# Kernel tuning notes

Hardware: AMD Instinct MI355X
Metric: run time of the kernel (lower is better)

Reference implementation:

```python
import jax, jax.numpy as jnp
import numpy as np

N = 10000       # nodes
E = 200000      # node pairs (edges) in rel_dict
R = 400000      # relation instances
F_IN = 128
F_OUT = 64


def setup_inputs() -> dict:
    key = jax.random.key(0)
    ks = jax.random.split(key, 8)
    x = jax.random.normal(ks[0], (N, F_IN), dtype=jnp.float32)
    rel = jax.random.normal(ks[1], (R, F_IN), dtype=jnp.float32)
    adj = jax.random.uniform(ks[2], (N, N), dtype=jnp.float32)
    edge_pairs = jax.random.randint(ks[3], (E, 2), 0, N, dtype=jnp.int32)
    rel_seg = jax.random.randint(ks[4], (R,), 0, E, dtype=jnp.int32)
    # Conv1d(in, out, kernel_size=1, bias=False) == Linear: weight [out, in]
    W = jax.random.normal(ks[5], (F_OUT, F_IN), dtype=jnp.float32) * 0.1
    w_rel = jax.random.normal(ks[6], (F_IN,), dtype=jnp.float32) * 0.1
    bias = jnp.zeros((F_OUT,), dtype=jnp.float32)
    return {"x": x, "rel": rel, "adj": adj, "edge_pairs": edge_pairs,
            "rel_seg": rel_seg, "W": W, "w_rel": w_rel, "bias": bias}


def reference(x, rel, adj, edge_pairs, rel_seg, W, w_rel, bias):
    # node transform: [N, F_OUT]
    seq_fts = x @ W.T
    # per-relation scalar: [R]
    fts_rel = rel @ w_rel
    # segment-mean per edge (vectorized form of the rel_dict loop)
    sums = jax.ops.segment_sum(fts_rel, rel_seg, num_segments=E)
    cnts = jax.ops.segment_sum(jnp.ones_like(fts_rel), rel_seg, num_segments=E)
    edge_means = sums / jnp.maximum(cnts, 1.0)  # [E]
    # symmetric scatter into dense logits [N, N]
    e1, e2 = edge_pairs[:, 0], edge_pairs[:, 1]
    logits = jnp.zeros_like(adj)
    logits = logits.at[e1, e2].set(edge_means).at[e2, e1].set(edge_means)
    # masked-ish softmax over rows, then sparse-weighted aggregation
    coefs = jax.nn.softmax(jax.nn.sigmoid(logits) + adj, axis=1)  # [N, N]
    # dropout is a no-op in eval mode (training=False)
    ret = coefs @ seq_fts + bias  # [N, F_OUT]
    return jax.nn.elu(ret)        # concat=True
```

## Files before the change

kernel.cpp:

```cpp
#include <hip/hip_runtime.h>
#include <math.h>

#define NN   10000
#define EE   200000
#define RR   400000
#define FIN  128
#define FOUT 64

#define HASH_BITS 20
#define HSIZE (1u << HASH_BITS)
#define HMASK (HSIZE - 1u)
#define ROWCAP 256

#define NKB 314
#define LDB 264

typedef __bf16 bf16x8 __attribute__((ext_vector_type(8)));
typedef __bf16 bf16x4 __attribute__((ext_vector_type(4)));
typedef float  f32x4  __attribute__((ext_vector_type(4)));

#define O_SUMS   0
#define O_CNTS   (O_SUMS + EE)
#define O_ROWCNT (O_CNTS + EE)
#define O_HKEY   (O_ROWCNT + NN)
#define O_HPRIO  (O_HKEY + HSIZE)
#define O_SEQTP  (O_HPRIO + HSIZE)
#define SEQTP_WORDS (NKB * 5 * 512 / 2)
#define ZERO_WORDS (O_SEQTP + SEQTP_WORDS)
#define O_NUMP   ZERO_WORDS
#define O_SP     (O_NUMP + 8 * NN * FOUT)
#define O_PAIRS  (O_SP + 8 * NN)

__global__ __launch_bounds__(256) void k_zero(f32x4* __restrict__ p, int n4) {
    int gid = blockIdx.x * 256 + threadIdx.x;
    if (gid < n4) p[gid] = (f32x4){0.f, 0.f, 0.f, 0.f};
}

__global__ __launch_bounds__(256) void k_seqfts(const float* __restrict__ x,
                                                const float* __restrict__ W,
                                                __bf16* __restrict__ seqTp) {
    __shared__ float Wt[FIN][FOUT + 1];
    __shared__ float xs[FIN][16 + 1];
    int t = threadIdx.x;
    for (int e = t; e < FOUT * FIN; e += 256) {
        int c = e >> 7, k = e & 127;
        Wt[k][c] = W[e];
    }
    int row0 = blockIdx.x * 16;
    for (int e = t; e < 16 * FIN; e += 256) {
        int r = e >> 7, k = e & 127;
        int gr = row0 + r;
        xs[k][r] = (gr < NN) ? x[(size_t)gr * FIN + k] : 0.f;
    }
    __syncthreads();
    int col = t & 63;
    int rg  = t >> 6;
    float acc[4] = {0.f, 0.f, 0.f, 0.f};
    for (int k = 0; k < FIN; ++k) {
        float w = Wt[k][col];
        #pragma unroll
        for (int i = 0; i < 4; ++i) acc[i] += w * xs[k][rg * 4 + i];
    }
    #pragma unroll
    for (int i = 0; i < 4; ++i) {
        int gr = row0 + rg * 4 + i;
        int kb = gr >> 5, g = (gr >> 3) & 3, slot = gr & 7;
        seqTp[((size_t)kb * 5 + (col >> 4)) * 512 + ((col & 15) + g * 16) * 8 + slot]
            = (__bf16)acc[i];
        if (col < 16)
            seqTp[((size_t)kb * 5 + 4) * 512 + (col + g * 16) * 8 + slot] = (__bf16)1.0f;
    }
}

__device__ __forceinline__ unsigned hash_cell(unsigned cell) {
    return (cell * 2654435761u) >> (32 - HASH_BITS);
}
__device__ __forceinline__ void entry_ij(const int* ep, int e, int& i, int& j, int& k) {
    k = (e < EE) ? e : e - EE;
    int a = ep[2 * k], b = ep[2 * k + 1];
    if (e < EE) { i = a; j = b; } else { i = b; j = a; }
}

#define KSPLIT 8
#define NSTRIP (NN / 16)
#define CPW 5
#define CHK 256
#define MAINW (NSTRIP * KSPLIT)
#define RELW  (RR / 16)
#define HASHW ((2 * EE + 63) / 64)
#define TOTW  (MAINW + RELW + HASHW)
#define GRID_MR ((TOTW + 3) / 4)

__global__ __launch_bounds__(256, 4) void k_mainrel(const float* __restrict__ adj,
                                                    const __bf16* __restrict__ seqTp,
                                                    const float* __restrict__ rel,
                                                    const float* __restrict__ wrel,
                                                    const int* __restrict__ rseg,
                                                    const int* __restrict__ ep,
                                                    float* __restrict__ sums,
                                                    float* __restrict__ cnts,
                                                    unsigned* __restrict__ hkey,
                                                    unsigned* __restrict__ hprio,
                                                    float* __restrict__ Nump,
                                                    float* __restrict__ Sp) {
    __shared__ __bf16 atile[4][16 * LDB];
    int t   = threadIdx.x;
    int wid = blockIdx.x * 4 + (t >> 6);
    int l   = t & 63;

    if (wid < MAINW) {
        int strip = wid >> 3;
        int ks    = wid & 7;
        int row0  = strip * 16;
        int lr = l & 15, lk = l >> 4;
        __bf16* my = &atile[t >> 6][0];

        f32x4 acc[5];
        #pragma unroll
        for (int n = 0; n < 5; ++n) acc[n] = (f32x4){0.f, 0.f, 0.f, 0.f};

        f32x4 pv[16];
        int c0 = ks * CPW;

        {
            int k0 = c0 * CHK;
            bool ok = (k0 + 4 * l) < NN;
            #pragma unroll
            for (int r = 0; r < 16; ++r) {
                f32x4 v = (f32x4){-1e9f, -1e9f, -1e9f, -1e9f};
                if (ok) v = *(const f32x4*)(adj + (size_t)(row0 + r) * NN + k0 + 4 * l);
                pv[r] = v;
            }
        }

        #pragma unroll
        for (int c = 0; c < CPW; ++c) {
            int k0 = (c0 + c) * CHK;
            #pragma unroll
            for (int r = 0; r < 16; ++r) {
                float e0 = exp2f(fmaf(pv[r].x, 1.442695041f, 0.7213475204f));
                float e1 = exp2f(fmaf(pv[r].y, 1.442695041f, 0.7213475204f));
                float e2 = exp2f(fmaf(pv[r].z, 1.442695041f, 0.7213475204f));
                float e3 = exp2f(fmaf(pv[r].w, 1.442695041f, 0.7213475204f));
                bf16x4 q = { (__bf16)e0, (__bf16)e1, (__bf16)e2, (__bf16)e3 };
                *(bf16x4*)&my[r * LDB + l * 4] = q;
            }
            if (c + 1 < CPW) {
                int kn = (c0 + c + 1) * CHK;
                bool ok = (kn + 4 * l) < NN;
                #pragma unroll
                for (int r = 0; r < 16; ++r) {
                    f32x4 v = (f32x4){-1e9f, -1e9f, -1e9f, -1e9f};
                    if (ok) v = *(const f32x4*)(adj + (size_t)(row0 + r) * NN + kn + 4 * l);
                    pv[r] = v;
                }
            }
            int kb0  = k0 >> 5;
            int hmax = min(8, (NN - k0 + 31) >> 5);
            for (int h = 0; h < hmax; ++h) {
                bf16x8 af = *(const bf16x8*)&my[lr * LDB + lk * 8 + h * 32];
                const __bf16* bp = seqTp + (size_t)(kb0 + h) * 5 * 512 + l * 8;
                #pragma unroll
                for (int n = 0; n < 5; ++n) {
                    bf16x8 b = *(const bf16x8*)(bp + n * 512);
                    acc[n] = __builtin_amdgcn_mfma_f32_16x16x32_bf16(af, b, acc[n], 0, 0, 0);
                }
            }
        }

        float* nout = Nump + (size_t)ks * NN * FOUT;
        #pragma unroll
        for (int n = 0; n < 4; ++n) {
            #pragma unroll
            for (int r = 0; r < 4; ++r)
                nout[(size_t)(row0 + lk * 4 + r) * FOUT + n * 16 + lr] = acc[n][r];
        }
        if (lr == 0) {
            #pragma unroll
            for (int r = 0; r < 4; ++r)
                Sp[(size_t)ks * NN + row0 + lk * 4 + r] = acc[4][r];
        }
        return;
    }

    if (wid < MAINW + RELW) {
        int rw   = wid - MAINW;
        int lane = l & 31;
        int half = l >> 5;
        f32x4 wv = *(const f32x4*)(wrel + lane * 4);
        #pragma unroll
        for (int it = 0; it < 8; ++it) {
            int row = rw * 16 + it * 2 + half;
            f32x4 v = *(const f32x4*)(rel + (size_t)row * FIN + lane * 4);
            float s = v.x * wv.x + v.y * wv.y + v.z * wv.z + v.w * wv.w;
            #pragma unroll
            for (int off = 16; off >= 1; off >>= 1) s += __shfl_xor(s, off, 64);
            if (lane == 0) {
                int seg = rseg[row];
                atomicAdd(&sums[seg], s);
                atomicAdd(&cnts[seg], 1.0f);
            }
        }
        return;
    }

    {
        int e = (wid - MAINW - RELW) * 64 + l;
        if (e >= 2 * EE) return;
        int i, j, k;
        entry_ij(ep, e, i, j, k);
        unsigned cell = (unsigned)i * NN + (unsigned)j;
        unsigned keyv = cell + 1u;
        unsigned h = hash_cell(cell);
        while (true) {
            unsigned old = atomicCAS(&hkey[h], 0u, keyv);
            if (old == 0u || old == keyv) break;
            h = (h + 1u) & HMASK;
        }
        atomicMax(&hprio[h], (unsigned)(e + 1));
    }
}

__global__ __launch_bounds__(256) void k_scatB(const int* __restrict__ ep,
                                               const float* __restrict__ sums,
                                               const float* __restrict__ cnts,
                                               const unsigned* __restrict__ hkey,
                                               const unsigned* __restrict__ hprio,
                                               const float* __restrict__ adj,
                                               int* __restrict__ rowcnt,
                                               uint2* __restrict__ pairs) {
    int e = blockIdx.x * 256 + threadIdx.x;
    if (e >= 2 * EE) return;
    int i, j, k;
    entry_ij(ep, e, i, j, k);
    unsigned cell = (unsigned)i * NN + (unsigned)j;
    unsigned keyv = cell + 1u;
    unsigned h = hash_cell(cell);
    while (hkey[h] != keyv) h = (h + 1u) & HMASK;
    if (hprio[h] == (unsigned)(e + 1)) {
        float v   = sums[k] / fmaxf(cnts[k], 1.0f);
        float sg  = 1.f / (1.f + __expf(-v));
        float aij = adj[(size_t)i * NN + j];
        float dw  = __expf(aij + sg) - __expf(aij + 0.5f);
        if (dw != 0.f) {
            int pos = atomicAdd(&rowcnt[i], 1);
            if (pos < ROWCAP)
                pairs[(size_t)i * ROWCAP + pos] =
                    make_uint2((unsigned)j, __float_as_uint(dw));
        }
    }
}

__global__ __launch_bounds__(256) void k_rowupd(const float* __restrict__ Nump,
                                                const float* __restrict__ Sp,
                                                const int* __restrict__ rowcnt,
                                                const uint2* __restrict__ pairs,
                                                const __bf16* __restrict__ seqTp,
                                                const float* __restrict__ bias,
                                                float* __restrict__ out) {
    int t = threadIdx.x;
    int i = blockIdx.x * 4 + (t >> 6);
    if (i >= NN) return;
    int c = t & 63;
    float acc = 0.f, sb = 0.f;
    #pragma unroll
    for (int ks = 0; ks < 8; ++ks) {
        acc += Nump[(size_t)ks * NN * FOUT + (size_t)i * FOUT + c];
        sb  += Sp[(size_t)ks * NN + i];
    }
    int cnt = min(rowcnt[i], ROWCAP);
    float sdw = 0.f;
    const uint2* pr = pairs + (size_t)i * ROWCAP;
    for (int e = 0; e < cnt; ++e) {
        uint2 pk = pr[e];
        float d  = __uint_as_float(pk.y);
        unsigned j = pk.x;
        float sj = (float)seqTp[((size_t)(j >> 5) * 5 + (c >> 4)) * 512
                                + ((c & 15) + ((j >> 3) & 3) * 16) * 8 + (j & 7)];
        acc += d * sj;
        sdw += d;
    }
    float v = acc / (sb + sdw) + bias[c];
    out[(size_t)i * FOUT + c] = (v > 0.f) ? v : expm1f(v);
}

extern "C" void kernel_launch(void* const* d_in, const int* in_sizes, int n_in,
                              void* d_out, int out_size, void* d_ws, size_t ws_size,
                              hipStream_t stream) {
    const float* x    = (const float*)d_in[0];
    const float* rel  = (const float*)d_in[1];
    const float* adj  = (const float*)d_in[2];
    const int*   ep   = (const int*)d_in[3];
    const int*   rseg = (const int*)d_in[4];
    const float* W    = (const float*)d_in[5];
    const float* wrel = (const float*)d_in[6];
    const float* bias = (const float*)d_in[7];
    float* out = (float*)d_out;

    float* ws = (float*)d_ws;
    float*    sums   = ws + O_SUMS;
    float*    cnts   = ws + O_CNTS;
    int*      rowcnt = (int*)(ws + O_ROWCNT);
    unsigned* hkey   = (unsigned*)(ws + O_HKEY);
    unsigned* hprio  = (unsigned*)(ws + O_HPRIO);
    __bf16*   seqTp  = (__bf16*)(ws + O_SEQTP);
    float*    Nump   = ws + O_NUMP;
    float*    Sp     = ws + O_SP;
    uint2*    pairs  = (uint2*)(ws + O_PAIRS);

    int n4 = ZERO_WORDS / 4;
    k_zero<<<(n4 + 255) / 256, 256, 0, stream>>>((f32x4*)d_ws, n4);
    k_seqfts<<<NN / 16, 256, 0, stream>>>(x, W, seqTp);
    k_mainrel<<<GRID_MR, 256, 0, stream>>>(adj, seqTp, rel, wrel, rseg, ep,
                                           sums, cnts, hkey, hprio, Nump, Sp);
    k_scatB<<<(2 * EE + 255) / 256, 256, 0, stream>>>(ep, sums, cnts, hkey, hprio,
                                                      adj, rowcnt, pairs);
    k_rowupd<<<(NN + 3) / 4, 256, 0, stream>>>(Nump, Sp, rowcnt, pairs,
                                               seqTp, bias, out);
}
```

Measured before the change: 320.0 us.

## Split fused main/rel/hash kernel into separate kernels with block-shared adj tiles

Splits the heterogeneous fused kernel into three launches: hash insertion, a grid-stride relation reduction, and a dense exp-matmul. In the new main kernel each block owns a 16-row strip; its four waves cooperatively load and exponentiate 512-column chunks into double-buffered shared memory and split the K range four ways. Partial outputs drop from 8 to 4 slices. The aim is less partial-sum traffic and better memory coalescing, at the cost of a __syncthreads per chunk, fewer concurrent waves per strip, and losing overlap between the irregular atomic work and the dense stream.

```diff
diff --git a/kernel.cpp b/kernel.cpp
--- a/kernel.cpp
+++ b/kernel.cpp
@@ -13,7 +13,9 @@
 #define ROWCAP 256
 
 #define NKB 314
-#define LDB 264
+#define NC  20
+#define CHKF 512
+#define LDSP 520
 
 typedef __bf16 bf16x8 __attribute__((ext_vector_type(8)));
 typedef __bf16 bf16x4 __attribute__((ext_vector_type(4)));
@@ -28,8 +30,8 @@
 #define SEQTP_WORDS (NKB * 5 * 512 / 2)
 #define ZERO_WORDS (O_SEQTP + SEQTP_WORDS)
 #define O_NUMP   ZERO_WORDS
-#define O_SP     (O_NUMP + 8 * NN * FOUT)
-#define O_PAIRS  (O_SP + 8 * NN)
+#define O_SP     (O_NUMP + 4 * NN * FOUT)
+#define O_PAIRS  (O_SP + 4 * NN)
 
 __global__ __launch_bounds__(256) void k_zero(f32x4* __restrict__ p, int n4) {
     int gid = blockIdx.x * 256 + threadIdx.x;
@@ -81,85 +83,109 @@
     if (e < EE) { i = a; j = b; } else { i = b; j = a; }
 }
 
-#define KSPLIT 8
-#define NSTRIP (NN / 16)
-#define CPW 5
-#define CHK 256
-#define MAINW (NSTRIP * KSPLIT)
-#define RELW  (RR / 16)
-#define HASHW ((2 * EE + 63) / 64)
-#define TOTW  (MAINW + RELW + HASHW)
-#define GRID_MR ((TOTW + 3) / 4)
-
-__global__ __launch_bounds__(256, 4) void k_mainrel(const float* __restrict__ adj,
-                                                    const __bf16* __restrict__ seqTp,
-                                                    const float* __restrict__ rel,
-                                                    const float* __restrict__ wrel,
-                                                    const int* __restrict__ rseg,
-                                                    const int* __restrict__ ep,
-                                                    float* __restrict__ sums,
-                                                    float* __restrict__ cnts,
-                                                    unsigned* __restrict__ hkey,
-                                                    unsigned* __restrict__ hprio,
-                                                    float* __restrict__ Nump,
-                                                    float* __restrict__ Sp) {
-    __shared__ __bf16 atile[4][16 * LDB];
-    int t   = threadIdx.x;
-    int wid = blockIdx.x * 4 + (t >> 6);
-    int l   = t & 63;
-
-    if (wid < MAINW) {
-        int strip = wid >> 3;
-        int ks    = wid & 7;
-        int row0  = strip * 16;
-        int lr = l & 15, lk = l >> 4;
-        __bf16* my = &atile[t >> 6][0];
-
-        f32x4 acc[5];
-        #pragma unroll
-        for (int n = 0; n < 5; ++n) acc[n] = (f32x4){0.f, 0.f, 0.f, 0.f};
-
-        f32x4 pv[16];
-        int c0 = ks * CPW;
-
-        {
-            int k0 = c0 * CHK;
-            bool ok = (k0 + 4 * l) < NN;
+__global__ __launch_bounds__(256) void k_hash(const int* __restrict__ ep,
+                                              unsigned* __restrict__ hkey,
+                                              unsigned* __restrict__ hprio) {
+    int e = blockIdx.x * 256 + threadIdx.x;
+    if (e >= 2 * EE) return;
+    int i, j, k;
+    entry_ij(ep, e, i, j, k);
+    unsigned cell = (unsigned)i * NN + (unsigned)j;
+    unsigned keyv = cell + 1u;
+    unsigned h = hash_cell(cell);
+    while (true) {
+        unsigned old = atomicCAS(&hkey[h], 0u, keyv);
+        if (old == 0u || old == keyv) break;
+        h = (h + 1u) & HMASK;
+    }
+    atomicMax(&hprio[h], (unsigned)(e + 1));
+}
+
+#define RELBLK 2048
+__global__ __launch_bounds__(256) void k_rel(const float* __restrict__ rel,
+                                             const float* __restrict__ wrel,
+                                             const int* __restrict__ rseg,
+                                             float* __restrict__ sums,
+                                             float* __restrict__ cnts) {
+    int t = threadIdx.x;
+    int wv = blockIdx.x * 4 + (t >> 6);
+    int l = t & 63;
+    int lane = l & 31, half = l >> 5;
+    f32x4 wvv = *(const f32x4*)(wrel + lane * 4);
+    const int NW2 = RELBLK * 4 * 2;
+    for (int base = wv * 2; base < RR; base += NW2) {
+        int row = base + half;
+        f32x4 v = *(const f32x4*)(rel + (size_t)row * FIN + lane * 4);
+        float s = v.x * wvv.x + v.y * wvv.y + v.z * wvv.z + v.w * wvv.w;
+        s += __shfl_xor(s, 1, 64);
+        s += __shfl_xor(s, 2, 64);
+        s += __shfl_xor(s, 4, 64);
+        s += __shfl_xor(s, 8, 64);
+        s += __shfl_xor(s, 16, 64);
+        if (lane == 0) {
+            int seg = rseg[row];
+            atomicAdd(&sums[seg], s);
+            atomicAdd(&cnts[seg], 1.0f);
+        }
+    }
+}
+
+__global__ __launch_bounds__(256) void k_main(const float* __restrict__ adj,
+                                              const __bf16* __restrict__ seqTp,
+                                              float* __restrict__ Nump,
+                                              float* __restrict__ Sp) {
+    __shared__ __bf16 As[2][16][LDSP];
+    int t = threadIdx.x;
+    int w = t >> 6, l = t & 63;
+    int row0 = blockIdx.x * 16;
+    int lr = l & 15, lk = l >> 4;
+
+    f32x4 acc[5];
+    #pragma unroll
+    for (int n = 0; n < 5; ++n) acc[n] = (f32x4){0.f, 0.f, 0.f, 0.f};
+
+    f32x4 pv[8];
+    #pragma unroll
+    for (int r = 0; r < 4; ++r) {
+        const float* ap = adj + (size_t)(row0 + w * 4 + r) * NN;
+        pv[2 * r]     = *(const f32x4*)(ap + 4 * l);
+        pv[2 * r + 1] = *(const f32x4*)(ap + 256 + 4 * l);
+    }
+
+    int p = 0;
+    for (int c = 0; c < NC; ++c) {
+        #pragma unroll
+        for (int r = 0; r < 4; ++r) {
             #pragma unroll
-            for (int r = 0; r < 16; ++r) {
-                f32x4 v = (f32x4){-1e9f, -1e9f, -1e9f, -1e9f};
-                if (ok) v = *(const f32x4*)(adj + (size_t)(row0 + r) * NN + k0 + 4 * l);
-                pv[r] = v;
+            for (int h2 = 0; h2 < 2; ++h2) {
+                f32x4 v = pv[2 * r + h2];
+                float e0 = exp2f(fmaf(v.x, 1.442695041f, 0.7213475204f));
+                float e1 = exp2f(fmaf(v.y, 1.442695041f, 0.7213475204f));
+                float e2 = exp2f(fmaf(v.z, 1.442695041f, 0.7213475204f));
+                float e3 = exp2f(fmaf(v.w, 1.442695041f, 0.7213475204f));
+                bf16x4 q = { (__bf16)e0, (__bf16)e1, (__bf16)e2, (__bf16)e3 };
+                *(bf16x4*)&As[p][w * 4 + r][h2 * 256 + 4 * l] = q;
             }
         }
-
-        #pragma unroll
-        for (int c = 0; c < CPW; ++c) {
-            int k0 = (c0 + c) * CHK;
+        if (c + 1 < NC) {
+            int kn = (c + 1) * CHKF;
             #pragma unroll
-            for (int r = 0; r < 16; ++r) {
-                float e0 = exp2f(fmaf(pv[r].x, 1.442695041f, 0.7213475204f));
-                float e1 = exp2f(fmaf(pv[r].y, 1.442695041f, 0.7213475204f));
-                float e2 = exp2f(fmaf(pv[r].z, 1.442695041f, 0.7213475204f));
-                float e3 = exp2f(fmaf(pv[r].w, 1.442695041f, 0.7213475204f));
-                bf16x4 q = { (__bf16)e0, (__bf16)e1, (__bf16)e2, (__bf16)e3 };
-                *(bf16x4*)&my[r * LDB + l * 4] = q;
+            for (int r = 0; r < 4; ++r) {
+                const float* ap = adj + (size_t)(row0 + w * 4 + r) * NN + kn;
+                pv[2 * r] = *(const f32x4*)(ap + 4 * l);
+                int g1 = kn + 256 + 4 * l;
+                pv[2 * r + 1] = (g1 < NN) ? *(const f32x4*)(ap + 256 + 4 * l)
+                                          : (f32x4){-1e9f, -1e9f, -1e9f, -1e9f};
             }
-            if (c + 1 < CPW) {
-                int kn = (c0 + c + 1) * CHK;
-                bool ok = (kn + 4 * l) < NN;
-                #pragma unroll
-                for (int r = 0; r < 16; ++r) {
-                    f32x4 v = (f32x4){-1e9f, -1e9f, -1e9f, -1e9f};
-                    if (ok) v = *(const f32x4*)(adj + (size_t)(row0 + r) * NN + kn + 4 * l);
-                    pv[r] = v;
-                }
-            }
-            int kb0  = k0 >> 5;
-            int hmax = min(8, (NN - k0 + 31) >> 5);
-            for (int h = 0; h < hmax; ++h) {
-                bf16x8 af = *(const bf16x8*)&my[lr * LDB + lk * 8 + h * 32];
-                const __bf16* bp = seqTp + (size_t)(kb0 + h) * 5 * 512 + l * 8;
+        }
+        __syncthreads();
+        int kb0 = (c * CHKF) >> 5;
+        #pragma unroll
+        for (int h = 0; h < 4; ++h) {
+            int kb = kb0 + w * 4 + h;
+            if (kb < NKB) {
+                bf16x8 af = *(const bf16x8*)&As[p][lr][w * 128 + h * 32 + lk * 8];
+                const __bf16* bp = seqTp + (size_t)kb * 5 * 512 + l * 8;
                 #pragma unroll
                 for (int n = 0; n < 5; ++n) {
                     bf16x8 b = *(const bf16x8*)(bp + n * 512);
@@ -167,57 +193,20 @@
                 }
             }
         }
-
-        float* nout = Nump + (size_t)ks * NN * FOUT;
-        #pragma unroll
-        for (int n = 0; n < 4; ++n) {
-            #pragma unroll
-            for (int r = 0; r < 4; ++r)
-                nout[(size_t)(row0 + lk * 4 + r) * FOUT + n * 16 + lr] = acc[n][r];
-        }
-        if (lr == 0) {
-            #pragma unroll
-            for (int r = 0; r < 4; ++r)
-                Sp[(size_t)ks * NN + row0 + lk * 4 + r] = acc[4][r];
-        }
-        return;
-    }
-
-    if (wid < MAINW + RELW) {
-        int rw   = wid - MAINW;
-        int lane = l & 31;
-        int half = l >> 5;
-        f32x4 wv = *(const f32x4*)(wrel + lane * 4);
-        #pragma unroll
-        for (int it = 0; it < 8; ++it) {
-            int row = rw * 16 + it * 2 + half;
-            f32x4 v = *(const f32x4*)(rel + (size_t)row * FIN + lane * 4);
-            float s = v.x * wv.x + v.y * wv.y + v.z * wv.z + v.w * wv.w;
-            #pragma unroll
-            for (int off = 16; off >= 1; off >>= 1) s += __shfl_xor(s, off, 64);
-            if (lane == 0) {
-                int seg = rseg[row];
-                atomicAdd(&sums[seg], s);
-                atomicAdd(&cnts[seg], 1.0f);
-            }
-        }
-        return;
-    }
-
-    {
-        int e = (wid - MAINW - RELW) * 64 + l;
-        if (e >= 2 * EE) return;
-        int i, j, k;
-        entry_ij(ep, e, i, j, k);
-        unsigned cell = (unsigned)i * NN + (unsigned)j;
-        unsigned keyv = cell + 1u;
-        unsigned h = hash_cell(cell);
-        while (true) {
-            unsigned old = atomicCAS(&hkey[h], 0u, keyv);
-            if (old == 0u || old == keyv) break;
-            h = (h + 1u) & HMASK;
-        }
-        atomicMax(&hprio[h], (unsigned)(e + 1));
+        p ^= 1;
+    }
+
+    float* nout = Nump + (size_t)w * NN * FOUT;
+    #pragma unroll
+    for (int n = 0; n < 4; ++n) {
+        #pragma unroll
+        for (int r = 0; r < 4; ++r)
+            nout[(size_t)(row0 + lk * 4 + r) * FOUT + n * 16 + lr] = acc[n][r];
+    }
+    if (lr == 0) {
+        #pragma unroll
+        for (int r = 0; r < 4; ++r)
+            Sp[(size_t)w * NN + row0 + lk * 4 + r] = acc[4][r];
     }
 }
 
@@ -264,7 +253,7 @@
     int c = t & 63;
     float acc = 0.f, sb = 0.f;
     #pragma unroll
-    for (int ks = 0; ks < 8; ++ks) {
+    for (int ks = 0; ks < 4; ++ks) {
         acc += Nump[(size_t)ks * NN * FOUT + (size_t)i * FOUT + c];
         sb  += Sp[(size_t)ks * NN + i];
     }
@@ -311,8 +300,9 @@
     int n4 = ZERO_WORDS / 4;
     k_zero<<<(n4 + 255) / 256, 256, 0, stream>>>((f32x4*)d_ws, n4);
     k_seqfts<<<NN / 16, 256, 0, stream>>>(x, W, seqTp);
-    k_mainrel<<<GRID_MR, 256, 0, stream>>>(adj, seqTp, rel, wrel, rseg, ep,
-                                           sums, cnts, hkey, hprio, Nump, Sp);
+    k_hash<<<(2 * EE + 255) / 256, 256, 0, stream>>>(ep, hkey, hprio);
+    k_rel<<<RELBLK, 256, 0, stream>>>(rel, wrel, rseg, sums, cnts);
+    k_main<<<NN / 16, 256, 0, stream>>>(adj, seqTp, Nump, Sp);
     k_scatB<<<(2 * EE + 255) / 256, 256, 0, stream>>>(ep, sums, cnts, hkey, hprio,
                                                       adj, rowcnt, pairs);
     k_rowupd<<<(NN + 3) / 4, 256, 0, stream>>>(Nump, Sp, rowcnt, pairs,
```

Result: no change. 315.6 us (-1.4%).
